# Kernel tuning notes

Measured on AMD Instinct MI355X. Metric: run time of the kernel, lower is better.

The kernel has to match this reference:

```python
import jax, jax.numpy as jnp
import numpy as np

B = 128          # batch
T = 196          # total_patches per view (2 views -> 2*T tokens)
ENC = 1024       # encoder_embed_dim
DEC = 512        # decoder_embed_dim
V = 98           # num unmasked (visible) tokens per sample
M = 2 * T - V    # num masked tokens (294)


def setup_inputs() -> dict:
    key = jax.random.key(0)
    kx, kperm, kw, kmt, kpos, kview = jax.random.split(key, 6)
    x = jax.random.normal(kx, (B, V, ENC), jnp.float32)
    # masked_ids: unique ids per row in [0, 2T) — built from permutations
    perms = jax.vmap(jax.random.permutation, in_axes=(0, None))(
        jax.random.split(kperm, B), 2 * T)
    masked_ids = perms[:, :M].astype(jnp.int64)
    W = jax.random.normal(kw, (DEC, ENC), jnp.float32) * 0.02
    b = jnp.zeros((DEC,), jnp.float32)
    mask_token = jax.random.normal(kmt, (1, 1, DEC), jnp.float32)
    pos_embed = jax.random.normal(kpos, (1, 2 * T, DEC), jnp.float32)
    view_embed = jax.random.normal(kview, (2, DEC), jnp.float32)
    return {"x": x, "masked_ids": masked_ids, "W": W, "b": b,
            "mask_token": mask_token, "pos_embed": pos_embed,
            "view_embed": view_embed}


def reference(x, masked_ids, W, b, mask_token, pos_embed, view_embed):
    Bn = x.shape[0]
    # Linear: enc -> dec
    xp = jnp.einsum('bve,de->bvd', x, W) + b          # (B, V, DEC)
    # visible ids = sorted complement of masked_ids (vectorized, no batch loop)
    rows = jnp.arange(Bn)[:, None]
    vis_mask = jnp.ones((Bn, 2 * T), bool).at[rows, masked_ids].set(False)
    # stable argsort puts True(visible, ~mask=False) positions first, in order
    visible_ids = jnp.argsort(~vis_mask, axis=1)[:, :V]  # (B, V)
    # scatter projected visible tokens into mask-token placeholders
    base = jnp.broadcast_to(mask_token, (Bn, 2 * T, DEC))
    view = base.at[rows, visible_ids].set(xp)          # (B, 2T, DEC)
    # per-view embedding: first T tokens -> view 0, last T -> view 1
    ve = jnp.concatenate([
        jnp.broadcast_to(view_embed[0], (T, DEC)),
        jnp.broadcast_to(view_embed[1], (T, DEC))], axis=0)  # (2T, DEC)
    return view + pos_embed + ve[None, :, :]
```

## Files before the change

### kernel.cpp

```cpp
#include <hip/hip_runtime.h>

#define BATCH 128
#define VIS   98
#define TOK   196
#define TOK2  392
#define ENC   1024
#define DEC   512
#define MSK   294

#define NXB 6272
#define NWB 256

typedef __bf16 bf16x8 __attribute__((ext_vector_type(8)));
typedef float  f32x4  __attribute__((ext_vector_type(4)));

__device__ __forceinline__ unsigned short f2bf(float f) {
    union { float f; unsigned u; } c; c.f = f;
    unsigned u = c.u;
    return (unsigned short)((u + 0x7fffu + ((u >> 16) & 1u)) >> 16);
}

__device__ __forceinline__ void g2lds16(const void* gptr, void* lptr) {
    __builtin_amdgcn_global_load_lds(
        (const __attribute__((address_space(1))) void*)gptr,
        (__attribute__((address_space(3))) void*)lptr, 16, 0, 0);
}

__global__ __launch_bounds__(512) void setup(const float* __restrict__ x,
                                             const float* __restrict__ W,
                                             const int* __restrict__ mids,
                                             unsigned short* __restrict__ xb,
                                             unsigned short* __restrict__ wbm,
                                             int* __restrict__ visids,
                                             unsigned char* __restrict__ flags) {
    int bid = blockIdx.x, tid = threadIdx.x;
    if (bid < NXB + NWB) {
        const float* src = (bid < NXB) ? x : W;
        unsigned short* dst = (bid < NXB) ? xb : wbm;
        int i = (bid < NXB ? bid : bid - NXB) * 512 + tid;
        float4 f = ((const float4*)src)[i];
        ushort4 o;
        o.x = f2bf(f.x); o.y = f2bf(f.y); o.z = f2bf(f.z); o.w = f2bf(f.w);
        ((ushort4*)dst)[i] = o;
        return;
    }
    int b = bid - NXB - NWB;
    __shared__ unsigned char lf[TOK2];
    __shared__ int wtot[8];
    if (tid < TOK2) lf[tid] = 1;
    __syncthreads();
    if (tid < MSK) lf[mids[b * MSK + tid]] = 0;
    __syncthreads();
    int flag = (tid < TOK2) ? (int)lf[tid] : 0;
    unsigned long long bal = __ballot(flag != 0);
    int lane = tid & 63, wv = tid >> 6;
    int pre = __popcll(bal & ((1ull << lane) - 1ull));
    if (lane == 0) wtot[wv] = __popcll(bal);
    __syncthreads();
    int off = 0;
    for (int i = 0; i < wv; ++i) off += wtot[i];
    if (flag) visids[b * VIS + off + pre] = tid;
    if (tid < TOK2) flags[b * TOK2 + tid] = lf[tid];
}

__global__ __launch_bounds__(256) void fill_masked(const unsigned char* __restrict__ flags,
                                                   const float* __restrict__ mask_token,
                                                   const float* __restrict__ pos,
                                                   const float* __restrict__ ve,
                                                   float* __restrict__ out) {
    int b = blockIdx.y;
    int g = blockIdx.x * 256 + threadIdx.x;
    int t  = g >> 7;
    int d4 = g & 127;
    int tok = b * TOK2 + t;
    if (flags[tok]) return;
    float4 m = ((const float4*)mask_token)[d4];
    float4 p = ((const float4*)(pos + (size_t)t * DEC))[d4];
    float4 v = ((const float4*)(ve + (t >= TOK ? DEC : 0)))[d4];
    float4 r;
    r.x = m.x + p.x + v.x;
    r.y = m.y + p.y + v.y;
    r.z = m.z + p.z + v.z;
    r.w = m.w + p.w + v.w;
    ((float4*)(out + (size_t)tok * DEC))[d4] = r;
}

__global__ __launch_bounds__(256, 4) void gemm_scatter(
    const unsigned short* __restrict__ xb,
    const unsigned short* __restrict__ wb,
    const float* __restrict__ bias,
    const float* __restrict__ pos,
    const float* __restrict__ ve,
    const int* __restrict__ vis,
    float* __restrict__ out) {
    __shared__ unsigned short As[64 * 64];
    __shared__ unsigned short Bs[128 * 64];
    __shared__ int rowdst[64];
    __shared__ int rowt[64];

    int tid = threadIdx.x;
    int lane = tid & 63, w = tid >> 6;
    int l16 = lane & 15, q = lane >> 4;
    int wm = w & 1, wn = w >> 1;
    int m0 = blockIdx.y * 64, n0 = blockIdx.x * 128;

    if (tid < 64) {
        int gr = m0 + tid;
        int t = vis[gr];
        rowt[tid] = t;
        rowdst[tid] = (gr / VIS) * TOK2 + t;
    }

    int c = (tid & 7) ^ ((tid >> 3) & 7);
    const unsigned short* gA = xb + (size_t)(m0 + (tid >> 3)) * ENC + c * 8;
    const unsigned short* gB = wb + (size_t)(n0 + (tid >> 3)) * ENC + c * 8;
    char* ldsA = (char*)As + tid * 16;
    char* ldsB = (char*)Bs + tid * 16;

    f32x4 acc[2][4];
    #pragma unroll
    for (int i = 0; i < 2; ++i)
        #pragma unroll
        for (int j = 0; j < 4; ++j)
            acc[i][j] = (f32x4){0.f, 0.f, 0.f, 0.f};

    for (int k0 = 0; k0 < ENC; k0 += 64) {
        __syncthreads();
        #pragma unroll
        for (int t = 0; t < 2; ++t)
            g2lds16(gA + (size_t)t * 32 * ENC + k0, ldsA + t * 4096);
        #pragma unroll
        for (int t = 0; t < 4; ++t)
            g2lds16(gB + (size_t)t * 32 * ENC + k0, ldsB + t * 4096);
        __syncthreads();

        #pragma unroll
        for (int u = 0; u < 2; ++u) {
            int slot = ((u * 4 + q) ^ (l16 & 7)) * 16;
            bf16x8 bfrag[4], afrag[2];
            #pragma unroll
            for (int j = 0; j < 4; ++j)
                bfrag[j] = *(const bf16x8*)((const char*)Bs + (wn * 64 + j * 16 + l16) * 128 + slot);
            #pragma unroll
            for (int i = 0; i < 2; ++i)
                afrag[i] = *(const bf16x8*)((const char*)As + (wm * 32 + i * 16 + l16) * 128 + slot);
            #pragma unroll
            for (int i = 0; i < 2; ++i)
                #pragma unroll
                for (int j = 0; j < 4; ++j)
                    acc[i][j] = __builtin_amdgcn_mfma_f32_16x16x32_bf16(afrag[i], bfrag[j], acc[i][j], 0, 0, 0);
        }
    }

    #pragma unroll
    for (int j = 0; j < 4; ++j) {
        int gcol = n0 + wn * 64 + j * 16 + l16;
        float bc = bias[gcol];
        float v0 = ve[gcol];
        float v1 = ve[DEC + gcol];
        #pragma unroll
        for (int i = 0; i < 2; ++i) {
            #pragma unroll
            for (int r = 0; r < 4; ++r) {
                int rl = wm * 32 + i * 16 + q * 4 + r;
                int t = rowt[rl];
                float val = acc[i][j][r] + bc + pos[(size_t)t * DEC + gcol]
                          + (t >= TOK ? v1 : v0);
                out[(size_t)rowdst[rl] * DEC + gcol] = val;
            }
        }
    }
}

extern "C" void kernel_launch(void* const* d_in, const int* in_sizes, int n_in,
                              void* d_out, int out_size, void* d_ws, size_t ws_size,
                              hipStream_t stream) {
    (void)in_sizes; (void)n_in; (void)out_size; (void)ws_size;
    const float* x    = (const float*)d_in[0];
    const int*   mids = (const int*)d_in[1];
    const float* W    = (const float*)d_in[2];
    const float* bias = (const float*)d_in[3];
    const float* mt   = (const float*)d_in[4];
    const float* pos  = (const float*)d_in[5];
    const float* ve   = (const float*)d_in[6];
    float* out = (float*)d_out;

    unsigned short* xb = (unsigned short*)d_ws;
    unsigned short* wbm = xb + (size_t)BATCH * VIS * ENC;
    int* visids = (int*)(wbm + (size_t)DEC * ENC);
    unsigned char* flags = (unsigned char*)(visids + BATCH * VIS);

    hipLaunchKernelGGL(setup, dim3(NXB + NWB + BATCH), dim3(512), 0, stream,
                       x, W, mids, xb, wbm, visids, flags);
    hipLaunchKernelGGL(fill_masked, dim3(TOK2 * 128 / 256, BATCH), dim3(256), 0, stream,
                       flags, mt, pos, ve, out);
    hipLaunchKernelGGL(gemm_scatter, dim3(4, (BATCH * VIS) / 64), dim3(256), 0, stream,
                       xb, wbm, bias, pos, ve, visids, out);
}
```

Baseline: 183.5 us.

## Fuse x bf16 conversion into GEMM loads and merge mask fill into GEMM launch

The separate pre-pass that converted x to bf16 in workspace is removed. The GEMM now streams fp32 x tiles directly into LDS with a swizzled layout and converts them to bf16 while building MFMA fragments. The masked-token fill kernel is folded into the same launch as extra blocks that loop over rows, saving one launch and one full round trip of x through memory. In exchange the A tile doubles in LDS size and adds per-fragment conversion ALU work, which may hurt occupancy.

```diff
diff --git a/kernel.cpp b/kernel.cpp
--- a/kernel.cpp
+++ b/kernel.cpp
@@ -8,8 +8,9 @@
 #define DEC   512
 #define MSK   294
 
-#define NXB 6272
 #define NWB 256
+#define GEMM_BLKS 784
+#define FILL_BLKS 240
 
 typedef __bf16 bf16x8 __attribute__((ext_vector_type(8)));
 typedef float  f32x4  __attribute__((ext_vector_type(4)));
@@ -20,31 +21,34 @@
     return (unsigned short)((u + 0x7fffu + ((u >> 16) & 1u)) >> 16);
 }
 
+__device__ __forceinline__ bf16x8 cvt8(f32x4 lo, f32x4 hi) {
+    bf16x8 r;
+    r[0] = (__bf16)lo[0]; r[1] = (__bf16)lo[1]; r[2] = (__bf16)lo[2]; r[3] = (__bf16)lo[3];
+    r[4] = (__bf16)hi[0]; r[5] = (__bf16)hi[1]; r[6] = (__bf16)hi[2]; r[7] = (__bf16)hi[3];
+    return r;
+}
+
 __device__ __forceinline__ void g2lds16(const void* gptr, void* lptr) {
     __builtin_amdgcn_global_load_lds(
         (const __attribute__((address_space(1))) void*)gptr,
         (__attribute__((address_space(3))) void*)lptr, 16, 0, 0);
 }
 
-__global__ __launch_bounds__(512) void setup(const float* __restrict__ x,
-                                             const float* __restrict__ W,
+__global__ __launch_bounds__(512) void setup(const float* __restrict__ W,
                                              const int* __restrict__ mids,
-                                             unsigned short* __restrict__ xb,
                                              unsigned short* __restrict__ wbm,
                                              int* __restrict__ visids,
                                              unsigned char* __restrict__ flags) {
     int bid = blockIdx.x, tid = threadIdx.x;
-    if (bid < NXB + NWB) {
-        const float* src = (bid < NXB) ? x : W;
-        unsigned short* dst = (bid < NXB) ? xb : wbm;
-        int i = (bid < NXB ? bid : bid - NXB) * 512 + tid;
-        float4 f = ((const float4*)src)[i];
+    if (bid < NWB) {
+        int i = bid * 512 + tid;
+        float4 f = ((const float4*)W)[i];
         ushort4 o;
         o.x = f2bf(f.x); o.y = f2bf(f.y); o.z = f2bf(f.z); o.w = f2bf(f.w);
-        ((ushort4*)dst)[i] = o;
+        ((ushort4*)wbm)[i] = o;
         return;
     }
-    int b = bid - NXB - NWB;
+    int b = bid - NWB;
     __shared__ unsigned char lf[TOK2];
     __shared__ int wtot[8];
     if (tid < TOK2) lf[tid] = 1;
@@ -63,46 +67,46 @@
     if (tid < TOK2) flags[b * TOK2 + tid] = lf[tid];
 }
 
-__global__ __launch_bounds__(256) void fill_masked(const unsigned char* __restrict__ flags,
-                                                   const float* __restrict__ mask_token,
-                                                   const float* __restrict__ pos,
-                                                   const float* __restrict__ ve,
-                                                   float* __restrict__ out) {
-    int b = blockIdx.y;
-    int g = blockIdx.x * 256 + threadIdx.x;
-    int t  = g >> 7;
-    int d4 = g & 127;
-    int tok = b * TOK2 + t;
-    if (flags[tok]) return;
-    float4 m = ((const float4*)mask_token)[d4];
-    float4 p = ((const float4*)(pos + (size_t)t * DEC))[d4];
-    float4 v = ((const float4*)(ve + (t >= TOK ? DEC : 0)))[d4];
-    float4 r;
-    r.x = m.x + p.x + v.x;
-    r.y = m.y + p.y + v.y;
-    r.z = m.z + p.z + v.z;
-    r.w = m.w + p.w + v.w;
-    ((float4*)(out + (size_t)tok * DEC))[d4] = r;
-}
-
-__global__ __launch_bounds__(256, 4) void gemm_scatter(
-    const unsigned short* __restrict__ xb,
+__global__ __launch_bounds__(256, 4) void gemm_fill(
+    const float* __restrict__ x,
     const unsigned short* __restrict__ wb,
     const float* __restrict__ bias,
+    const float* __restrict__ mask_token,
     const float* __restrict__ pos,
     const float* __restrict__ ve,
     const int* __restrict__ vis,
+    const unsigned char* __restrict__ flags,
     float* __restrict__ out) {
-    __shared__ unsigned short As[64 * 64];
+    __shared__ float          As[64 * 64];
     __shared__ unsigned short Bs[128 * 64];
     __shared__ int rowdst[64];
     __shared__ int rowt[64];
 
-    int tid = threadIdx.x;
+    int bid = blockIdx.x, tid = threadIdx.x;
+
+    if (bid >= GEMM_BLKS) {
+        int fb = bid - GEMM_BLKS;
+        int d4 = tid & 127, sub = tid >> 7;
+        float4 m = ((const float4*)mask_token)[d4];
+        for (int row = fb * 2 + sub; row < BATCH * TOK2; row += FILL_BLKS * 2) {
+            if (flags[row]) continue;
+            int t = row % TOK2;
+            float4 p = ((const float4*)(pos + (size_t)t * DEC))[d4];
+            float4 v = ((const float4*)(ve + (t >= TOK ? DEC : 0)))[d4];
+            float4 r;
+            r.x = m.x + p.x + v.x;
+            r.y = m.y + p.y + v.y;
+            r.z = m.z + p.z + v.z;
+            r.w = m.w + p.w + v.w;
+            ((float4*)(out + (size_t)row * DEC))[d4] = r;
+        }
+        return;
+    }
+
     int lane = tid & 63, w = tid >> 6;
     int l16 = lane & 15, q = lane >> 4;
     int wm = w & 1, wn = w >> 1;
-    int m0 = blockIdx.y * 64, n0 = blockIdx.x * 128;
+    int n0 = (bid & 3) * 128, m0 = (bid >> 2) * 64;
 
     if (tid < 64) {
         int gr = m0 + tid;
@@ -111,9 +115,12 @@
         rowdst[tid] = (gr / VIS) * TOK2 + t;
     }
 
-    int c = (tid & 7) ^ ((tid >> 3) & 7);
-    const unsigned short* gA = xb + (size_t)(m0 + (tid >> 3)) * ENC + c * 8;
-    const unsigned short* gB = wb + (size_t)(n0 + (tid >> 3)) * ENC + c * 8;
+    int rA = tid >> 4;
+    int cA = (tid & 15) ^ (rA & 15);
+    const float* gA = x + (size_t)(m0 + rA) * ENC + cA * 4;
+    int rB = tid >> 3;
+    int cB = (tid & 7) ^ (rB & 7);
+    const unsigned short* gB = wb + (size_t)(n0 + rB) * ENC + cB * 8;
     char* ldsA = (char*)As + tid * 16;
     char* ldsB = (char*)Bs + tid * 16;
 
@@ -127,8 +134,8 @@
     for (int k0 = 0; k0 < ENC; k0 += 64) {
         __syncthreads();
         #pragma unroll
-        for (int t = 0; t < 2; ++t)
-            g2lds16(gA + (size_t)t * 32 * ENC + k0, ldsA + t * 4096);
+        for (int t = 0; t < 4; ++t)
+            g2lds16(gA + (size_t)t * 16 * ENC + k0, ldsA + t * 4096);
         #pragma unroll
         for (int t = 0; t < 4; ++t)
             g2lds16(gB + (size_t)t * 32 * ENC + k0, ldsB + t * 4096);
@@ -136,14 +143,21 @@
 
         #pragma unroll
         for (int u = 0; u < 2; ++u) {
-            int slot = ((u * 4 + q) ^ (l16 & 7)) * 16;
-            bf16x8 bfrag[4], afrag[2];
+            int slotB = ((u * 4 + q) ^ (l16 & 7)) * 16;
+            bf16x8 bfrag[4];
             #pragma unroll
             for (int j = 0; j < 4; ++j)
-                bfrag[j] = *(const bf16x8*)((const char*)Bs + (wn * 64 + j * 16 + l16) * 128 + slot);
-            #pragma unroll
-            for (int i = 0; i < 2; ++i)
-                afrag[i] = *(const bf16x8*)((const char*)As + (wm * 32 + i * 16 + l16) * 128 + slot);
+                bfrag[j] = *(const bf16x8*)((const char*)Bs + (wn * 64 + j * 16 + l16) * 128 + slotB);
+            bf16x8 afrag[2];
+            #pragma unroll
+            for (int i = 0; i < 2; ++i) {
+                int ar = wm * 32 + i * 16 + l16;
+                int p0 = ((u * 8 + 2 * q) ^ l16) * 16;
+                int p1 = ((u * 8 + 2 * q + 1) ^ l16) * 16;
+                f32x4 lo = *(const f32x4*)((const char*)As + ar * 256 + p0);
+                f32x4 hi = *(const f32x4*)((const char*)As + ar * 256 + p1);
+                afrag[i] = cvt8(lo, hi);
+            }
             #pragma unroll
             for (int i = 0; i < 2; ++i)
                 #pragma unroll
@@ -185,15 +199,12 @@
     const float* ve   = (const float*)d_in[6];
     float* out = (float*)d_out;
 
-    unsigned short* xb = (unsigned short*)d_ws;
-    unsigned short* wbm = xb + (size_t)BATCH * VIS * ENC;
+    unsigned short* wbm = (unsigned short*)d_ws;
     int* visids = (int*)(wbm + (size_t)DEC * ENC);
     unsigned char* flags = (unsigned char*)(visids + BATCH * VIS);
 
-    hipLaunchKernelGGL(setup, dim3(NXB + NWB + BATCH), dim3(512), 0, stream,
-                       x, W, mids, xb, wbm, visids, flags);
-    hipLaunchKernelGGL(fill_masked, dim3(TOK2 * 128 / 256, BATCH), dim3(256), 0, stream,
-                       flags, mt, pos, ve, out);
-    hipLaunchKernelGGL(gemm_scatter, dim3(4, (BATCH * VIS) / 64), dim3(256), 0, stream,
-                       xb, wbm, bias, pos, ve, visids, out);
-}
+    hipLaunchKernelGGL(setup, dim3(NWB + BATCH), dim3(512), 0, stream,
+                       W, mids, wbm, visids, flags);
+    hipLaunchKernelGGL(gemm_fill, dim3(GEMM_BLKS + FILL_BLKS), dim3(256), 0, stream,
+                       x, wbm, bias, mt, pos, ve, visids, flags, out);
+}
```

New measurement: 204.4 us. 1.11x slower.
